# Kernel tuning notes

Hardware: AMD Instinct MI355X
Metric: run time of the kernel (lower is better)

## Reference

```python
import jax, jax.numpy as jnp
import numpy as np

N, DIN, DOUT = 8192, 2048, 2048


def setup_inputs() -> dict:
    key = jax.random.key(0)
    k1, k2, k3 = jax.random.split(key, 3)
    x = jax.random.normal(k1, (N, DIN), dtype=jnp.float32)
    # quantized params: uint8 kernel, uint16 bias (as produced by model.quantize)
    qkernel = jax.random.randint(k2, (DIN, DOUT), 0, 256, dtype=jnp.int32).astype(jnp.uint8)
    qbias = jax.random.randint(k3, (DOUT,), 0, 65536, dtype=jnp.int32).astype(jnp.uint16)
    scale = jnp.array(0.5, dtype=jnp.float32)
    zero_point = jnp.array(0.5, dtype=jnp.float32)
    return {"x": x, "scale": scale, "zero_point": zero_point,
            "qkernel": qkernel, "qbias": qbias}


def reference(x, scale, zero_point, qkernel, qbias) -> jnp.ndarray:
    # quantize(x, b=8, uint8): clip(round(x/scale) + zero_point, 0, 255)
    qmax = 2 ** 8 - 1
    xq = jnp.clip(jnp.round(x / scale) + zero_point, 0, qmax).astype(jnp.uint8)
    acc = jnp.dot(xq, qkernel, preferred_element_type=jnp.uint16)
    acc = (acc + qbias).astype(jnp.uint32)  # uint16 add wraps, then widen
    # dequantize: (x - zero_point) * scale  -> float32
    return (acc - zero_point) * scale
```

## Files before the change

kernel.cpp:

```cpp
#include <hip/hip_runtime.h>
#include <stdint.h>


#define NROWS 8192
#define DIN   2048
#define DOUT  2048

typedef int v4i __attribute__((ext_vector_type(4)));

__device__ inline void gload16(const uint8_t* g, uint8_t* l) {
  __builtin_amdgcn_global_load_lds(
      (__attribute__((address_space(1))) void*)(g),
      (__attribute__((address_space(3))) void*)(l), 16, 0, 0);
}

__device__ inline void wgbar() {
  __builtin_amdgcn_sched_barrier(0);
  __builtin_amdgcn_s_barrier();
  __builtin_amdgcn_sched_barrier(0);
}

__device__ inline uint32_t q4(float4 v, float s, float z, int& sum) {
  uint32_t w = 0;
  float e[4] = {v.x, v.y, v.z, v.w};
#pragma unroll
  for (int i = 0; i < 4; ++i) {
    float tq = rintf(e[i] / s) + z;
    tq = fminf(fmaxf(tq, 0.0f), 255.0f);
    uint32_t q = (uint32_t)tq;
    sum += (int)q;
    w |= ((q ^ 0x80u) & 0xFFu) << (8 * i);
  }
  return w;
}

__global__ __launch_bounds__(256) void kq(const float* __restrict__ x,
                                          const float* __restrict__ sp,
                                          const float* __restrict__ zpp,
                                          uint8_t* __restrict__ xq,
                                          int* __restrict__ rs128,
                                          int* __restrict__ ccomb) {
  const int row = blockIdx.x;
  const int t = threadIdx.x;
  if (row == 0) {
#pragma unroll
    for (int i = 0; i < DOUT / 256; ++i) ccomb[i * 256 + t] = 0;
  }
  const float s = sp[0], z = zpp[0];
  const float4* xr = (const float4*)(x + (size_t)row * DIN);
  float4 a = xr[t];
  float4 b = xr[t + 256];
  int sum = 0;
  uint32_t w0 = q4(a, s, z, sum);
  uint32_t w1 = q4(b, s, z, sum);
  uint32_t* xw = (uint32_t*)(xq + (size_t)row * DIN);
  xw[t] = w0;
  xw[t + 256] = w1;
#pragma unroll
  for (int o = 32; o > 0; o >>= 1) sum += __shfl_down(sum, o);
  __shared__ int ws4[4];
  if ((t & 63) == 0) ws4[t >> 6] = sum;
  __syncthreads();
  if (t == 0) rs128[row] = 128 * (ws4[0] + ws4[1] + ws4[2] + ws4[3]);
}

__global__ __launch_bounds__(256) void kt(const void* __restrict__ qk,
                                          const void* __restrict__ qbias,
                                          uint8_t* __restrict__ qkT,
                                          int* __restrict__ ccomb) {
  __shared__ uint8_t tile[64][68];
  __shared__ int sflag;
  const int t = threadIdx.x;
  if (t == 0) sflag = 0;
  __syncthreads();
  {
    const int* q32 = (const int*)qk;
    int bad = 0;
#pragma unroll
    for (int i = 0; i < 4; ++i) bad |= ((unsigned)q32[t + 256 * i] > 255u);
    if (bad) sflag = 1;
  }
  __syncthreads();
  const int u8mode = sflag;

  const int n0 = blockIdx.x * 64;
  const int k0 = blockIdx.y * 64;
  const int tx = t & 15;
  const int ty = t >> 4;
  if (u8mode) {
    const uint8_t* q8 = (const uint8_t*)qk;
#pragma unroll
    for (int j = 0; j < 4; ++j) {
      int r = j * 16 + ty;
      uint32_t w = *(const uint32_t*)(q8 + (size_t)(k0 + r) * DOUT + n0 + tx * 4);
      tile[r][tx * 4 + 0] = (uint8_t)(w & 255u);
      tile[r][tx * 4 + 1] = (uint8_t)((w >> 8) & 255u);
      tile[r][tx * 4 + 2] = (uint8_t)((w >> 16) & 255u);
      tile[r][tx * 4 + 3] = (uint8_t)((w >> 24) & 255u);
    }
  } else {
    const int* q32 = (const int*)qk;
#pragma unroll
    for (int j = 0; j < 4; ++j) {
      int r = j * 16 + ty;
      int4 w = *(const int4*)(q32 + (size_t)(k0 + r) * DOUT + n0 + tx * 4);
      tile[r][tx * 4 + 0] = (uint8_t)w.x;
      tile[r][tx * 4 + 1] = (uint8_t)w.y;
      tile[r][tx * 4 + 2] = (uint8_t)w.z;
      tile[r][tx * 4 + 3] = (uint8_t)w.w;
    }
  }
  __syncthreads();
#pragma unroll
  for (int j = 0; j < 4; ++j) {
    int r = j * 16 + ty;
    uint32_t b0 = tile[tx * 4 + 0][r];
    uint32_t b1 = tile[tx * 4 + 1][r];
    uint32_t b2 = tile[tx * 4 + 2][r];
    uint32_t b3 = tile[tx * 4 + 3][r];
    *(uint32_t*)(qkT + (size_t)(n0 + r) * DIN + k0 + tx * 4) =
        (b0 ^ 0x80u) | ((b1 ^ 0x80u) << 8) | ((b2 ^ 0x80u) << 16) | ((b3 ^ 0x80u) << 24);
    int part = (int)(b0 + b1 + b2 + b3);
#pragma unroll
    for (int m = 1; m < 16; m <<= 1) part += __shfl_xor(part, m);
    if (tx == 0) atomicAdd(&ccomb[n0 + r], part << 7);
  }
  if (blockIdx.y == 0 && t < 64) {
    int n = n0 + t;
    int qb = u8mode ? (int)((const uint16_t*)qbias)[n] : ((const int*)qbias)[n];
    atomicAdd(&ccomb[n], qb);
  }
}

__global__ __launch_bounds__(512, 2) void kg(const uint8_t* __restrict__ A,
                                             const uint8_t* __restrict__ B,
                                             const int* __restrict__ rs128,
                                             const int* __restrict__ ccomb,
                                             const float* __restrict__ sp,
                                             const float* __restrict__ zpp,
                                             float* __restrict__ out) {
  __shared__ __align__(16) uint8_t lds[131072];
  const int t = threadIdx.x;
  const int l = t & 63, wid = t >> 6;
  const int wr = wid >> 2, wc = wid & 3;
  const int rl = l & 15, kgp = l >> 4;

  const int bid = blockIdx.x;
  const int swz = (bid & 7) * 32 + (bid >> 3);
  const int m0 = (swz >> 3) * 256;
  const int n0 = (swz & 7) * 256;

  const int srow = t >> 2;
  const int sc = (t & 3) ^ (srow & 3);
  const uint8_t* gA = A + (size_t)(m0 + srow) * DIN + sc * 16;
  const uint8_t* gA2 = gA + (size_t)128 * DIN;
  const uint8_t* gB = B + (size_t)(n0 + srow) * DIN + sc * 16;
  const uint8_t* gB2 = gB + (size_t)128 * DIN;
  const int sdst = t * 16;

#define STAGE_A(BUF, KS, KB) do {                                   \
    uint8_t* d_ = lds + (BUF) * 32768 + (KS) * 16384 + sdst;        \
    gload16(gA + (KB) + (KS) * 64, d_);                             \
    gload16(gA2 + (KB) + (KS) * 64, d_ + 8192);                     \
  } while (0)
#define STAGE_B(BUF, KS, KB) do {                                   \
    uint8_t* d_ = lds + 65536 + (BUF) * 32768 + (KS) * 16384 + sdst;\
    gload16(gB + (KB) + (KS) * 64, d_);                             \
    gload16(gB2 + (KB) + (KS) * 64, d_ + 8192);                     \
  } while (0)

  const int aoff0 = (wr * 128 + rl) * 64 + ((kgp ^ (rl & 3)) << 4);
  const int boff0 = 65536 + (wc * 64 + rl) * 64 + ((kgp ^ (rl & 3)) << 4);

  v4i acc[8][4];
#pragma unroll
  for (int i = 0; i < 8; ++i)
#pragma unroll
    for (int j = 0; j < 4; ++j) acc[i][j] = (v4i){0, 0, 0, 0};
  v4i af[4], bf[4];

#define LD_A(MH, KH) do {                                            \
    const uint8_t* ap_ = lds + cur * 32768 + (KH) * 16384 + aoff0 + (MH) * 4096; \
    _Pragma("unroll")                                                \
    for (int q = 0; q < 4; ++q) af[q] = *(const v4i*)(ap_ + q * 1024);\
  } while (0)
#define LD_B(KH) do {                                                \
    const uint8_t* bp_ = lds + cur * 32768 + (KH) * 16384 + boff0;   \
    _Pragma("unroll")                                                \
    for (int nj = 0; nj < 4; ++nj) bf[nj] = *(const v4i*)(bp_ + nj * 1024); \
  } while (0)
#define DO_MFMA(MH) do {                                             \
    __builtin_amdgcn_s_setprio(1);                                   \
    _Pragma("unroll")                                                \
    for (int q = 0; q < 4; ++q)                                      \
      _Pragma("unroll")                                              \
      for (int nj = 0; nj < 4; ++nj)                                 \
        acc[(MH) * 4 + q][nj] = __builtin_amdgcn_mfma_i32_16x16x64_i8(\
            af[q], bf[nj], acc[(MH) * 4 + q][nj], 0, 0, 0);          \
    __builtin_amdgcn_s_setprio(0);                                   \
  } while (0)

  STAGE_A(0, 0, 0);
  STAGE_B(0, 0, 0);
  STAGE_A(0, 1, 0);
  STAGE_B(0, 1, 0);

  int cur = 0;
  for (int tt = 0; tt < 16; ++tt) {
    const int nb = cur ^ 1;
    const int kn = ((tt + 1) & 15) * 128;
    asm volatile("s_waitcnt vmcnt(4)" ::: "memory");
    wgbar();
    LD_B(0);
    LD_A(0, 0);
    STAGE_A(nb, 0, kn);
    DO_MFMA(0);
    wgbar();
    LD_A(1, 0);
    STAGE_B(nb, 0, kn);
    DO_MFMA(1);
    asm volatile("s_waitcnt vmcnt(4)" ::: "memory");
    wgbar();
    LD_B(1);
    LD_A(0, 1);
    STAGE_A(nb, 1, kn);
    DO_MFMA(0);
    wgbar();
    LD_A(1, 1);
    STAGE_B(nb, 1, kn);
    DO_MFMA(1);
    cur = nb;
  }

  const float s = sp[0], z = zpp[0];
  int cc[4];
#pragma unroll
  for (int nj = 0; nj < 4; ++nj) cc[nj] = ccomb[n0 + wc * 64 + nj * 16 + rl];
#pragma unroll
  for (int mi = 0; mi < 8; ++mi) {
#pragma unroll
    for (int r = 0; r < 4; ++r) {
      int row = m0 + wr * 128 + mi * 16 + kgp * 4 + r;
      int rs = rs128[row];
#pragma unroll
      for (int nj = 0; nj < 4; ++nj) {
        int col = n0 + wc * 64 + nj * 16 + rl;
        uint32_t v = (uint32_t)(acc[mi][nj][r] + rs + cc[nj]) & 0xFFFFu;
        out[(size_t)row * DOUT + col] = ((float)v - z) * s;
      }
    }
  }
#undef STAGE_A
#undef STAGE_B
#undef LD_A
#undef LD_B
#undef DO_MFMA
}

extern "C" void kernel_launch(void* const* d_in, const int* in_sizes, int n_in,
                              void* d_out, int out_size, void* d_ws, size_t ws_size,
                              hipStream_t stream) {
  const float* x   = (const float*)d_in[0];
  const float* sp  = (const float*)d_in[1];
  const float* zpp = (const float*)d_in[2];
  const void*  qk  = d_in[3];
  const void*  qb  = d_in[4];
  float* out = (float*)d_out;

  uint8_t* ws = (uint8_t*)d_ws;
  uint8_t* xq  = ws;
  uint8_t* qkT = ws + (16u << 20);
  int* rs128 = (int*)(ws + (20u << 20));
  int* ccomb = (int*)(ws + (20u << 20) + (32u << 10));

  kq<<<NROWS, 256, 0, stream>>>(x, sp, zpp, xq, rs128, ccomb);
  kt<<<dim3(DOUT / 64, DIN / 64), 256, 0, stream>>>(qk, qb, qkT, ccomb);
  kg<<<dim3(256), 512, 0, stream>>>(xq, qkT, rs128, ccomb, sp, zpp, out);
}
```

Measured before the change: 164.0 us.

## Fuse quantize and transpose prologue kernels; compute column sums with MFMA in GEMM

Merges the activation-quantize and weight-transpose kernels into a single launch, so one kernel boundary and the ccomb zeroing and atomics disappear. Column sums of the weights are now computed inside the GEMM by extra MFMAs against an all-ones vector, instead of with shuffle reductions and atomicAdd in the transpose. The change also alters the LDS swizzle pattern to reduce bank conflicts and replaces the division by scale with a reciprocal multiply. The extra MFMAs add tensor work to every k-step, and the reciprocal multiply can round differently from the original division.

```diff
diff --git a/kernel.cpp b/kernel.cpp
--- a/kernel.cpp
+++ b/kernel.cpp
@@ -20,12 +20,12 @@
   __builtin_amdgcn_sched_barrier(0);
 }
 
-__device__ inline uint32_t q4(float4 v, float s, float z, int& sum) {
+__device__ inline uint32_t q4(float4 v, float inv, float z, int& sum) {
   uint32_t w = 0;
   float e[4] = {v.x, v.y, v.z, v.w};
 #pragma unroll
   for (int i = 0; i < 4; ++i) {
-    float tq = rintf(e[i] / s) + z;
+    float tq = rintf(e[i] * inv) + z;
     tq = fminf(fmaxf(tq, 0.0f), 255.0f);
     uint32_t q = (uint32_t)tq;
     sum += (int)q;
@@ -34,43 +34,39 @@
   return w;
 }
 
-__global__ __launch_bounds__(256) void kq(const float* __restrict__ x,
+__global__ __launch_bounds__(256) void kp(const float* __restrict__ x,
                                           const float* __restrict__ sp,
                                           const float* __restrict__ zpp,
+                                          const void* __restrict__ qk,
+                                          const void* __restrict__ qbias,
                                           uint8_t* __restrict__ xq,
                                           int* __restrict__ rs128,
-                                          int* __restrict__ ccomb) {
-  const int row = blockIdx.x;
+                                          uint8_t* __restrict__ qkT,
+                                          int* __restrict__ qb32) {
   const int t = threadIdx.x;
-  if (row == 0) {
-#pragma unroll
-    for (int i = 0; i < DOUT / 256; ++i) ccomb[i * 256 + t] = 0;
-  }
-  const float s = sp[0], z = zpp[0];
-  const float4* xr = (const float4*)(x + (size_t)row * DIN);
-  float4 a = xr[t];
-  float4 b = xr[t + 256];
-  int sum = 0;
-  uint32_t w0 = q4(a, s, z, sum);
-  uint32_t w1 = q4(b, s, z, sum);
-  uint32_t* xw = (uint32_t*)(xq + (size_t)row * DIN);
-  xw[t] = w0;
-  xw[t + 256] = w1;
-#pragma unroll
-  for (int o = 32; o > 0; o >>= 1) sum += __shfl_down(sum, o);
-  __shared__ int ws4[4];
-  if ((t & 63) == 0) ws4[t >> 6] = sum;
-  __syncthreads();
-  if (t == 0) rs128[row] = 128 * (ws4[0] + ws4[1] + ws4[2] + ws4[3]);
-}
-
-__global__ __launch_bounds__(256) void kt(const void* __restrict__ qk,
-                                          const void* __restrict__ qbias,
-                                          uint8_t* __restrict__ qkT,
-                                          int* __restrict__ ccomb) {
+  if (blockIdx.x < NROWS) {
+    const int row = blockIdx.x;
+    const float s = sp[0], z = zpp[0];
+    const float inv = 1.0f / s;
+    const float4* xr = (const float4*)(x + (size_t)row * DIN);
+    float4 a = xr[t];
+    float4 b = xr[t + 256];
+    int sum = 0;
+    uint32_t w0 = q4(a, inv, z, sum);
+    uint32_t w1 = q4(b, inv, z, sum);
+    uint32_t* xw = (uint32_t*)(xq + (size_t)row * DIN);
+    xw[t] = w0;
+    xw[t + 256] = w1;
+#pragma unroll
+    for (int o = 32; o > 0; o >>= 1) sum += __shfl_down(sum, o);
+    __shared__ int ws4[4];
+    if ((t & 63) == 0) ws4[t >> 6] = sum;
+    __syncthreads();
+    if (t == 0) rs128[row] = 128 * (ws4[0] + ws4[1] + ws4[2] + ws4[3]);
+    return;
+  }
   __shared__ uint8_t tile[64][68];
   __shared__ int sflag;
-  const int t = threadIdx.x;
   if (t == 0) sflag = 0;
   __syncthreads();
   {
@@ -83,15 +79,16 @@
   __syncthreads();
   const int u8mode = sflag;
 
-  const int n0 = blockIdx.x * 64;
-  const int k0 = blockIdx.y * 64;
+  const int j = blockIdx.x - NROWS;
+  const int n0 = (j & 31) * 64;
+  const int k0 = (j >> 5) * 64;
   const int tx = t & 15;
   const int ty = t >> 4;
   if (u8mode) {
     const uint8_t* q8 = (const uint8_t*)qk;
 #pragma unroll
-    for (int j = 0; j < 4; ++j) {
-      int r = j * 16 + ty;
+    for (int jj = 0; jj < 4; ++jj) {
+      int r = jj * 16 + ty;
       uint32_t w = *(const uint32_t*)(q8 + (size_t)(k0 + r) * DOUT + n0 + tx * 4);
       tile[r][tx * 4 + 0] = (uint8_t)(w & 255u);
       tile[r][tx * 4 + 1] = (uint8_t)((w >> 8) & 255u);
@@ -101,8 +98,8 @@
   } else {
     const int* q32 = (const int*)qk;
 #pragma unroll
-    for (int j = 0; j < 4; ++j) {
-      int r = j * 16 + ty;
+    for (int jj = 0; jj < 4; ++jj) {
+      int r = jj * 16 + ty;
       int4 w = *(const int4*)(q32 + (size_t)(k0 + r) * DOUT + n0 + tx * 4);
       tile[r][tx * 4 + 0] = (uint8_t)w.x;
       tile[r][tx * 4 + 1] = (uint8_t)w.y;
@@ -112,30 +109,25 @@
   }
   __syncthreads();
 #pragma unroll
-  for (int j = 0; j < 4; ++j) {
-    int r = j * 16 + ty;
+  for (int jj = 0; jj < 4; ++jj) {
+    int r = jj * 16 + ty;
     uint32_t b0 = tile[tx * 4 + 0][r];
     uint32_t b1 = tile[tx * 4 + 1][r];
     uint32_t b2 = tile[tx * 4 + 2][r];
     uint32_t b3 = tile[tx * 4 + 3][r];
     *(uint32_t*)(qkT + (size_t)(n0 + r) * DIN + k0 + tx * 4) =
         (b0 ^ 0x80u) | ((b1 ^ 0x80u) << 8) | ((b2 ^ 0x80u) << 16) | ((b3 ^ 0x80u) << 24);
-    int part = (int)(b0 + b1 + b2 + b3);
-#pragma unroll
-    for (int m = 1; m < 16; m <<= 1) part += __shfl_xor(part, m);
-    if (tx == 0) atomicAdd(&ccomb[n0 + r], part << 7);
-  }
-  if (blockIdx.y == 0 && t < 64) {
+  }
+  if (k0 == 0 && t < 64) {
     int n = n0 + t;
-    int qb = u8mode ? (int)((const uint16_t*)qbias)[n] : ((const int*)qbias)[n];
-    atomicAdd(&ccomb[n], qb);
+    qb32[n] = u8mode ? (int)((const uint16_t*)qbias)[n] : ((const int*)qbias)[n];
   }
 }
 
 __global__ __launch_bounds__(512, 2) void kg(const uint8_t* __restrict__ A,
                                              const uint8_t* __restrict__ B,
                                              const int* __restrict__ rs128,
-                                             const int* __restrict__ ccomb,
+                                             const int* __restrict__ qb32,
                                              const float* __restrict__ sp,
                                              const float* __restrict__ zpp,
                                              float* __restrict__ out) {
@@ -151,7 +143,7 @@
   const int n0 = (swz & 7) * 256;
 
   const int srow = t >> 2;
-  const int sc = (t & 3) ^ (srow & 3);
+  const int sc = (t & 3) ^ ((srow >> 1) & 3);
   const uint8_t* gA = A + (size_t)(m0 + srow) * DIN + sc * 16;
   const uint8_t* gA2 = gA + (size_t)128 * DIN;
   const uint8_t* gB = B + (size_t)(n0 + srow) * DIN + sc * 16;
@@ -169,14 +161,19 @@
     gload16(gB2 + (KB) + (KS) * 64, d_ + 8192);                     \
   } while (0)
 
-  const int aoff0 = (wr * 128 + rl) * 64 + ((kgp ^ (rl & 3)) << 4);
-  const int boff0 = 65536 + (wc * 64 + rl) * 64 + ((kgp ^ (rl & 3)) << 4);
+  const int swl = (rl >> 1) & 3;
+  const int aoff0 = (wr * 128 + rl) * 64 + ((kgp ^ swl) << 4);
+  const int boff0 = 65536 + (wc * 64 + rl) * 64 + ((kgp ^ swl) << 4);
 
   v4i acc[8][4];
 #pragma unroll
   for (int i = 0; i < 8; ++i)
 #pragma unroll
     for (int j = 0; j < 4; ++j) acc[i][j] = (v4i){0, 0, 0, 0};
+  v4i csum[4];
+#pragma unroll
+  for (int j = 0; j < 4; ++j) csum[j] = (v4i){0, 0, 0, 0};
+  const v4i ones = (v4i){0x01010101, 0x01010101, 0x01010101, 0x01010101};
   v4i af[4], bf[4];
 
 #define LD_A(MH, KH) do {                                            \
@@ -199,6 +196,12 @@
             af[q], bf[nj], acc[(MH) * 4 + q][nj], 0, 0, 0);          \
     __builtin_amdgcn_s_setprio(0);                                   \
   } while (0)
+#define DO_CSUM() do {                                               \
+    _Pragma("unroll")                                                \
+    for (int nj = 0; nj < 4; ++nj)                                   \
+      csum[nj] = __builtin_amdgcn_mfma_i32_16x16x64_i8(              \
+          ones, bf[nj], csum[nj], 0, 0, 0);                          \
+  } while (0)
 
   STAGE_A(0, 0, 0);
   STAGE_B(0, 0, 0);
@@ -215,6 +218,7 @@
     LD_A(0, 0);
     STAGE_A(nb, 0, kn);
     DO_MFMA(0);
+    DO_CSUM();
     wgbar();
     LD_A(1, 0);
     STAGE_B(nb, 0, kn);
@@ -225,6 +229,7 @@
     LD_A(0, 1);
     STAGE_A(nb, 1, kn);
     DO_MFMA(0);
+    DO_CSUM();
     wgbar();
     LD_A(1, 1);
     STAGE_B(nb, 1, kn);
@@ -235,7 +240,7 @@
   const float s = sp[0], z = zpp[0];
   int cc[4];
 #pragma unroll
-  for (int nj = 0; nj < 4; ++nj) cc[nj] = ccomb[n0 + wc * 64 + nj * 16 + rl];
+  for (int nj = 0; nj < 4; ++nj) cc[nj] = (csum[nj][0] << 7) + qb32[n0 + wc * 64 + nj * 16 + rl];
 #pragma unroll
   for (int mi = 0; mi < 8; ++mi) {
 #pragma unroll
@@ -255,6 +260,7 @@
 #undef LD_A
 #undef LD_B
 #undef DO_MFMA
+#undef DO_CSUM
 }
 
 extern "C" void kernel_launch(void* const* d_in, const int* in_sizes, int n_in,
@@ -271,9 +277,9 @@
   uint8_t* xq  = ws;
   uint8_t* qkT = ws + (16u << 20);
   int* rs128 = (int*)(ws + (20u << 20));
-  int* ccomb = (int*)(ws + (20u << 20) + (32u << 10));
-
-  kq<<<NROWS, 256, 0, stream>>>(x, sp, zpp, xq, rs128, ccomb);
-  kt<<<dim3(DOUT / 64, DIN / 64), 256, 0, stream>>>(qk, qb, qkT, ccomb);
-  kg<<<dim3(256), 512, 0, stream>>>(xq, qkT, rs128, ccomb, sp, zpp, out);
-}
+  int* qb32  = (int*)(ws + (20u << 20) + (32u << 10));
+
+  kp<<<NROWS + (DIN / 64) * (DOUT / 64), 256, 0, stream>>>(
+      x, sp, zpp, qk, qb, xq, rs128, qkT, qb32);
+  kg<<<dim3(256), 512, 0, stream>>>(xq, qkT, rs128, qb32, sp, zpp, out);
+}
```

Result: no change. 160.9 us (-1.9%).
